# Performance work log

Measured on AMD Instinct MI355X. Metric: run time of the kernel, lower is better.

Reference implementation:

```python
import jax, jax.numpy as jnp
import numpy as np

DIM = 1024
DIM_HEAD = 64
HEADS = 16
INNER = DIM_HEAD * HEADS
SCALE = 8.0
EPS_LN = 1e-5
EPS_L2 = 1e-12


def _layernorm(x, gamma):
    mu = jnp.mean(x, axis=-1, keepdims=True)
    var = jnp.var(x, axis=-1, keepdims=True)
    return (x - mu) / jnp.sqrt(var + EPS_LN) * gamma  # beta is a zero buffer


def _l2norm(t):
    n = jnp.linalg.norm(t, axis=-1, keepdims=True)
    return t / jnp.maximum(n, EPS_L2)


def setup_inputs() -> dict:
    key = jax.random.key(0)
    ks = jax.random.split(key, 8)
    b, n = 4, 2048
    x = jax.random.normal(ks[0], (b, n, DIM), dtype=jnp.float32)
    context_mask = jax.random.randint(ks[1], (b, n), 0, 2) > 0
    gamma = jnp.ones((DIM,), dtype=jnp.float32)
    wq = jax.random.normal(ks[2], (DIM, INNER), dtype=jnp.float32) * 0.02
    wkv = jax.random.normal(ks[3], (DIM, 2 * INNER), dtype=jnp.float32) * 0.02
    null_kv = jax.random.normal(ks[4], (2, HEADS, 1, DIM_HEAD), dtype=jnp.float32)
    q_scale = jnp.ones((DIM_HEAD,), dtype=jnp.float32)
    k_scale = jnp.ones((DIM_HEAD,), dtype=jnp.float32)
    wo = jax.random.normal(ks[5], (INNER, DIM), dtype=jnp.float32) * 0.02
    return {"x": x, "context_mask": context_mask, "gamma": gamma, "wq": wq,
            "wkv": wkv, "null_kv": null_kv, "q_scale": q_scale,
            "k_scale": k_scale, "wo": wo}


def reference(x, context_mask, gamma, wq, wkv, null_kv, q_scale, k_scale, wo):
    b, n, _ = x.shape
    xn = _layernorm(x, gamma)
    q = xn @ wq                     # [b, n, inner]
    kv = xn @ wkv                   # self-attention: kv_input = x
    k, v = jnp.split(kv, 2, axis=-1)

    def split_heads(t):
        return t.reshape(b, n, HEADS, DIM_HEAD).transpose(0, 2, 1, 3)  # b h n d

    q, k, v = map(split_heads, (q, k, v))
    nk = jnp.broadcast_to(null_kv[0][None], (b, HEADS, 1, DIM_HEAD))
    nv = jnp.broadcast_to(null_kv[1][None], (b, HEADS, 1, DIM_HEAD))
    k = jnp.concatenate([nk, k], axis=2)  # b h (n+1) d
    v = jnp.concatenate([nv, v], axis=2)

    q = _l2norm(q) * q_scale
    k = _l2norm(k) * k_scale

    sim = jnp.einsum('bhid,bhjd->bhij', q, k) * SCALE  # b h n (n+1)
    mask = jnp.pad(context_mask, ((0, 0), (1, 0)), constant_values=True)  # null kv always visible
    mask_value = -jnp.finfo(sim.dtype).max
    sim = jnp.where(mask[:, None, None, :], sim, mask_value)

    attn = jax.nn.softmax(sim, axis=-1)
    out = jnp.einsum('bhij,bhjd->bhid', attn, v)
    out = out.transpose(0, 2, 1, 3).reshape(b, n, INNER)
    return out @ wo
```

## Files before the change

### kernel.cpp

```cpp
#include <hip/hip_runtime.h>

typedef unsigned short u16;
typedef unsigned int u32;
typedef unsigned long long u64;
typedef __bf16 bf16x8 __attribute__((ext_vector_type(8)));
typedef float f32x4 __attribute__((ext_vector_type(4)));

#define B_ 4
#define N_ 2048
#define D_ 1024
#define H_ 16
#define DH_ 64
#define NKP_ 2112
#define NKT_ 33

__device__ __forceinline__ float bf2f(u16 u) {
  union { u32 i; float f; } v; v.i = ((u32)u) << 16; return v.f;
}
__device__ __forceinline__ u16 f2bf(float f) {
  union { float f; u32 i; } v; v.f = f;
  u32 r = v.i + 0x7fffu + ((v.i >> 16) & 1u);
  return (u16)(r >> 16);
}
__device__ __forceinline__ u32 cvtpk(float a, float b) {
  u32 r;
  asm("v_cvt_pk_bf16_f32 %0, %1, %2" : "=v"(r) : "v"(a), "v"(b));
  return r;
}
__device__ __forceinline__ void load_lds16(const void* g, void* l) {
  __builtin_amdgcn_global_load_lds((const __attribute__((address_space(1))) void*)g,
                                   (__attribute__((address_space(3))) void*)l, 16, 0, 0);
}

__global__ __launch_bounds__(256) void ln_kernel(const float* __restrict__ x,
                                                 const float* __restrict__ gamma,
                                                 u16* __restrict__ xn) {
  int row = blockIdx.x;
  int tid = threadIdx.x, lane = tid & 63, wid = tid >> 6;
  const float4 v = ((const float4*)(x + (size_t)row * D_))[tid];
  float s  = v.x + v.y + v.z + v.w;
  float ss = v.x * v.x + v.y * v.y + v.z * v.z + v.w * v.w;
#pragma unroll
  for (int off = 1; off < 64; off <<= 1) {
    s  += __shfl_xor(s,  off, 64);
    ss += __shfl_xor(ss, off, 64);
  }
  __shared__ float rs[4], rss[4];
  if (lane == 0) { rs[wid] = s; rss[wid] = ss; }
  __syncthreads();
  float S  = rs[0] + rs[1] + rs[2] + rs[3];
  float SS = rss[0] + rss[1] + rss[2] + rss[3];
  float mean = S * (1.0f / D_);
  float var  = SS * (1.0f / D_) - mean * mean;
  float inv  = rsqrtf(var + 1e-5f);
  const float4 g = ((const float4*)gamma)[tid];
  u16* o = xn + (size_t)row * D_ + tid * 4;
  o[0] = f2bf((v.x - mean) * inv * g.x);
  o[1] = f2bf((v.y - mean) * inv * g.y);
  o[2] = f2bf((v.z - mean) * inv * g.z);
  o[3] = f2bf((v.w - mean) * inv * g.w);
}

__global__ __launch_bounds__(256) void wt_kernel(const float* __restrict__ W,
                                                 u16* __restrict__ WT,
                                                 int K, int N) {
  __shared__ float t[32][33];
  int tiles_n = N >> 5;
  int tk = blockIdx.x / tiles_n, tn = blockIdx.x % tiles_n;
  int tx = threadIdx.x & 31, ty = threadIdx.x >> 5;
  int k0 = tk << 5, n0 = tn << 5;
#pragma unroll
  for (int i = 0; i < 4; ++i)
    t[ty + i * 8][tx] = W[(size_t)(k0 + ty + i * 8) * N + n0 + tx];
  __syncthreads();
#pragma unroll
  for (int i = 0; i < 4; ++i)
    WT[(size_t)(n0 + ty + i * 8) * K + k0 + tx] = f2bf(t[tx][ty + i * 8]);
}

__global__ __launch_bounds__(256) void prep_kernel(const int* __restrict__ mask,
                                                   const float* __restrict__ qs,
                                                   const float* __restrict__ ksc,
                                                   const float* __restrict__ null_kv,
                                                   u16* __restrict__ Kb,
                                                   u16* __restrict__ Vt,
                                                   u64* __restrict__ km,
                                                   float* __restrict__ cb) {
  int bh = blockIdx.x, h = bh & 15;
  int tid = threadIdx.x, lane = tid & 63, wid = tid >> 6;
  if (wid == 0) {
    float kv = null_kv[h * 64 + lane];
    float ss = kv * kv;
#pragma unroll
    for (int off = 1; off < 64; off <<= 1) ss += __shfl_xor(ss, off, 64);
    float inv = 1.0f / fmaxf(sqrtf(ss), 1e-12f);
    Kb[((size_t)bh * NKP_ + 2048) * 64 + lane] = f2bf(kv * inv * ksc[lane]);
    Vt[((size_t)bh * 64 + lane) * NKP_ + 2048] = f2bf(null_kv[1024 + h * 64 + lane]);
  }
  for (int i = tid; i < 63 * 64; i += 256) {
    int r = i >> 6, c = i & 63;
    Kb[((size_t)bh * NKP_ + 2049 + r) * 64 + c] = 0;
  }
  for (int i = tid; i < 64 * 63; i += 256) {
    int d = i / 63, c = i % 63;
    Vt[((size_t)bh * 64 + d) * NKP_ + 2049 + c] = 0;
  }
  if (bh == 0) {
    if (tid < B_ * NKT_) {
      int b = tid / NKT_, kt = tid % NKT_;
      u64 m = 0;
      if (kt < 32) {
#pragma unroll 8
        for (int jj = 0; jj < 64; ++jj)
          m |= (u64)(mask[b * N_ + kt * 64 + jj] != 0) << jj;
      } else {
        m = 1ull;
      }
      km[tid] = m;
    }
    if (tid == 0) {
      float mw = 0.f;
      for (int i = 0; i < DH_; ++i) mw = fmaxf(mw, fabsf(qs[i] * ksc[i]));
      cb[0] = -8.0f * mw * 1.4426950408889634f;
    }
  }
}

template <int MODE>
__global__ __launch_bounds__(256) void gemm_bt(const u16* __restrict__ A,
                                               const u16* __restrict__ Bt,
                                               void* __restrict__ Cv,
                                               int M, int N, int K,
                                               const float* __restrict__ qs,
                                               u16* __restrict__ Vt) {
  __shared__ __attribute__((aligned(16))) u16 sm[2 * 128 * 64];
  u16* a_sm = sm;
  u16* b_sm = sm + 128 * 64;
  int tid = threadIdx.x, lane = tid & 63, wid = tid >> 6;
  int m0 = blockIdx.x * 128, n0 = blockIdx.y * 128;
  int wm = (wid >> 1) * 64, wn = (wid & 1) * 64;
  int sr = lane >> 3, sc = (lane & 7) * 8;
  int la = lane & 15, lk = (lane >> 4) * 8;
  f32x4 acc[4][4] = {};
  for (int k0 = 0; k0 < K; k0 += 64) {
    __syncthreads();
#pragma unroll
    for (int i = 0; i < 4; ++i) {
      int r = i * 32 + wid * 8;
      load_lds16(A  + (size_t)(m0 + r + sr) * K + k0 + sc, &a_sm[r * 64]);
      load_lds16(Bt + (size_t)(n0 + r + sr) * K + k0 + sc, &b_sm[r * 64]);
    }
    __syncthreads();
#pragma unroll
    for (int s = 0; s < 2; ++s) {
      bf16x8 af[4], bfr[4];
#pragma unroll
      for (int mf = 0; mf < 4; ++mf)
        af[mf] = *(const bf16x8*)&a_sm[(wm + mf * 16 + la) * 64 + s * 32 + lk];
#pragma unroll
      for (int nf = 0; nf < 4; ++nf)
        bfr[nf] = *(const bf16x8*)&b_sm[(wn + nf * 16 + la) * 64 + s * 32 + lk];
#pragma unroll
      for (int mf = 0; mf < 4; ++mf)
#pragma unroll
        for (int nf = 0; nf < 4; ++nf)
          acc[mf][nf] = __builtin_amdgcn_mfma_f32_16x16x32_bf16(af[mf], bfr[nf], acc[mf][nf], 0, 0, 0);
    }
  }
  int crow = (lane >> 4) * 4, ccol = lane & 15;

  if (MODE == 3) {
    int by = blockIdx.y;
    int rr0 = m0 + wm;
    int b = rr0 >> 11;
    int seq0 = rr0 & 2047;
    if (by < 8) {
      int h = by * 2 + (wn >> 6);
      float kscv[4];
#pragma unroll
      for (int nf = 0; nf < 4; ++nf) kscv[nf] = qs[nf * 16 + ccol];
      u16* kb = (u16*)Cv + ((size_t)(b * 16 + h) * NKP_) * 64;
#pragma unroll
      for (int mf = 0; mf < 4; ++mf) {
        float invr[4];
#pragma unroll
        for (int r = 0; r < 4; ++r) {
          float ss = 0.f;
#pragma unroll
          for (int nf = 0; nf < 4; ++nf) ss += acc[mf][nf][r] * acc[mf][nf][r];
#pragma unroll
          for (int off = 1; off < 16; off <<= 1) ss += __shfl_xor(ss, off, 64);
          invr[r] = 1.0f / fmaxf(sqrtf(ss), 1e-12f);
        }
#pragma unroll
        for (int nf = 0; nf < 4; ++nf)
#pragma unroll
          for (int r = 0; r < 4; ++r)
            kb[(size_t)(seq0 + mf * 16 + crow + r) * 64 + nf * 16 + ccol] =
                f2bf(acc[mf][nf][r] * invr[r] * kscv[nf]);
      }
    } else {
      int h = (by - 8) * 2 + (wn >> 6);
      __syncthreads();
      u16* tw = sm + wid * 4096;
#pragma unroll
      for (int mf = 0; mf < 4; ++mf)
#pragma unroll
        for (int nf = 0; nf < 4; ++nf) {
          int row = nf * 16 + ccol;
#pragma unroll
          for (int r = 0; r < 4; ++r)
            tw[row * 64 + ((mf * 16 + crow + r) ^ ((row & 7) * 8))] = f2bf(acc[mf][nf][r]);
        }
      u16* vb = Vt + ((size_t)(b * 16 + h) * 64) * NKP_;
      int dr = lane >> 3, kc = (lane & 7) * 8;
#pragma unroll
      for (int i = 0; i < 8; ++i) {
        int d = i * 8 + dr;
        bf16x8 vv = *(const bf16x8*)&tw[d * 64 + (kc ^ ((d & 7) * 8))];
        *(bf16x8*)(vb + (size_t)d * NKP_ + seq0 + kc) = vv;
      }
    }
    return;
  }

  float qsv[4];
  if (MODE == 2) {
#pragma unroll
    for (int nf = 0; nf < 4; ++nf) qsv[nf] = qs[nf * 16 + ccol];
  }
#pragma unroll
  for (int mf = 0; mf < 4; ++mf) {
    float invr[4];
    if (MODE == 2) {
#pragma unroll
      for (int r = 0; r < 4; ++r) {
        float ss = 0.f;
#pragma unroll
        for (int nf = 0; nf < 4; ++nf) ss += acc[mf][nf][r] * acc[mf][nf][r];
#pragma unroll
        for (int off = 1; off < 16; off <<= 1) ss += __shfl_xor(ss, off, 64);
        invr[r] = 1.0f / fmaxf(sqrtf(ss), 1e-12f);
      }
    }
#pragma unroll
    for (int nf = 0; nf < 4; ++nf) {
      int rr = m0 + wm + mf * 16 + crow;
      int cc = n0 + wn + nf * 16 + ccol;
      if (MODE == 1) {
        float* C = (float*)Cv;
#pragma unroll
        for (int r = 0; r < 4; ++r) C[(size_t)(rr + r) * N + cc] = acc[mf][nf][r];
      } else if (MODE == 0) {
        u16* C = (u16*)Cv;
#pragma unroll
        for (int r = 0; r < 4; ++r) C[(size_t)(rr + r) * N + cc] = f2bf(acc[mf][nf][r]);
      } else {
        u16* C = (u16*)Cv;
#pragma unroll
        for (int r = 0; r < 4; ++r)
          C[(size_t)(rr + r) * N + cc] = f2bf(acc[mf][nf][r] * invr[r] * qsv[nf]);
      }
    }
  }
}

__global__ __launch_bounds__(512) void attn_kernel(const u16* __restrict__ Q,
                                                   const u16* __restrict__ Kb,
                                                   const u16* __restrict__ Vt,
                                                   const u64* __restrict__ km,
                                                   const float* __restrict__ cb,
                                                   u16* __restrict__ O) {
  __shared__ __attribute__((aligned(16))) u16 k_sm[2][64 * 64];
  __shared__ __attribute__((aligned(16))) u16 v_sm[2][64 * 64];
  __shared__ __attribute__((aligned(16))) u16 p_sm[8][32 * 64];
  int tid = threadIdx.x, lane = tid & 63, wid = tid >> 6;
  int bh = blockIdx.x, b = bh >> 4, h = bh & 15;
  int q0 = blockIdx.y * 256 + wid * 32;
  int la = lane & 15, lk = (lane >> 4) * 8, crow = (lane >> 4) * 4;
  int swz = (la & 7) * 8;
  int sr = lane >> 3;
  int scz = ((lane & 7) ^ (lane >> 3)) * 8;

  bf16x8 aq[2][2];
#pragma unroll
  for (int qb = 0; qb < 2; ++qb) {
    const u16* qrow = Q + ((size_t)(b * N_) + q0 + qb * 16 + la) * D_ + h * DH_;
#pragma unroll
    for (int s = 0; s < 2; ++s) aq[qb][s] = *(const bf16x8*)(qrow + s * 32 + lk);
  }
  float l[2] = {0.f, 0.f};
  f32x4 o[2][4] = {};
  const u16* Kbh = Kb + (size_t)bh * NKP_ * 64;
  const u16* Vbh = Vt + (size_t)bh * 64 * NKP_;
  const u64* kmb = km + (size_t)b * NKT_;
  const float C1 = 11.541560327111707f;
  const float cbias = cb[0];

#define STAGE(bb, kt)                                                          \
  do {                                                                         \
    int key0_ = (kt) * 64;                                                     \
    int r_ = wid * 8;                                                          \
    load_lds16(Kbh + (size_t)(key0_ + r_ + sr) * 64 + scz, &k_sm[bb][r_ * 64]); \
    load_lds16(Vbh + (size_t)(r_ + sr) * NKP_ + key0_ + scz, &v_sm[bb][r_ * 64]); \
  } while (0)

  STAGE(0, 0);

  for (int kt = 0; kt < NKT_; ++kt) {
    int bb = kt & 1;
    __syncthreads();
    if (kt + 1 < NKT_) STAGE(bb ^ 1, kt + 1);
    u64 kmv = kmb[kt];

    f32x4 sacc[2][4] = {};
    __builtin_amdgcn_s_setprio(1);
#pragma unroll
    for (int nf = 0; nf < 4; ++nf) {
      bf16x8 bk0 = *(const bf16x8*)&k_sm[bb][(nf * 16 + la) * 64 + (lk ^ swz)];
      bf16x8 bk1 = *(const bf16x8*)&k_sm[bb][(nf * 16 + la) * 64 + ((32 + lk) ^ swz)];
#pragma unroll
      for (int qb = 0; qb < 2; ++qb) {
        sacc[qb][nf] = __builtin_amdgcn_mfma_f32_16x16x32_bf16(bk0, aq[qb][0], sacc[qb][nf], 0, 0, 0);
        sacc[qb][nf] = __builtin_amdgcn_mfma_f32_16x16x32_bf16(bk1, aq[qb][1], sacc[qb][nf], 0, 0, 0);
      }
    }
    __builtin_amdgcn_s_setprio(0);

#pragma unroll
    for (int nf = 0; nf < 4; ++nf) {
      u32 nib = ((u32)(kmv >> (nf * 16 + crow))) & 0xFu;
      int key = nf * 16 + crow;
#pragma unroll
      for (int qb = 0; qb < 2; ++qb) {
        float p0 = __builtin_amdgcn_exp2f(fmaf(sacc[qb][nf][0], C1, cbias));
        float p1 = __builtin_amdgcn_exp2f(fmaf(sacc[qb][nf][1], C1, cbias));
        float p2 = __builtin_amdgcn_exp2f(fmaf(sacc[qb][nf][2], C1, cbias));
        float p3 = __builtin_amdgcn_exp2f(fmaf(sacc[qb][nf][3], C1, cbias));
        p0 = (nib & 1u) ? p0 : 0.f;
        p1 = (nib & 2u) ? p1 : 0.f;
        p2 = (nib & 4u) ? p2 : 0.f;
        p3 = (nib & 8u) ? p3 : 0.f;
        l[qb] += (p0 + p1) + (p2 + p3);
        int row = qb * 16 + la;
        *(u32*)&p_sm[wid][row * 64 + (key ^ swz)] = cvtpk(p0, p1);
        *(u32*)&p_sm[wid][row * 64 + ((key + 2) ^ swz)] = cvtpk(p2, p3);
      }
    }

    __builtin_amdgcn_s_setprio(1);
#pragma unroll
    for (int s = 0; s < 2; ++s) {
      bf16x8 bv[4];
#pragma unroll
      for (int dt = 0; dt < 4; ++dt)
        bv[dt] = *(const bf16x8*)&v_sm[bb][(dt * 16 + la) * 64 + ((s * 32 + lk) ^ swz)];
#pragma unroll
      for (int qb = 0; qb < 2; ++qb) {
        bf16x8 ap = *(const bf16x8*)&p_sm[wid][(qb * 16 + la) * 64 + ((s * 32 + lk) ^ swz)];
#pragma unroll
        for (int dt = 0; dt < 4; ++dt)
          o[qb][dt] = __builtin_amdgcn_mfma_f32_16x16x32_bf16(ap, bv[dt], o[qb][dt], 0, 0, 0);
      }
    }
    __builtin_amdgcn_s_setprio(0);
  }
#undef STAGE

#pragma unroll
  for (int qb = 0; qb < 2; ++qb) {
    l[qb] += __shfl_xor(l[qb], 16, 64);
    l[qb] += __shfl_xor(l[qb], 32, 64);
#pragma unroll
    for (int r = 0; r < 4; ++r) {
      float lq = __shfl(l[qb], crow + r, 64);
      float inv = 1.0f / lq;
      int n = q0 + qb * 16 + crow + r;
      u16* ob = O + ((size_t)(b * N_) + n) * D_ + h * DH_;
#pragma unroll
      for (int dt = 0; dt < 4; ++dt) ob[dt * 16 + la] = f2bf(o[qb][dt][r] * inv);
    }
  }
}

extern "C" void kernel_launch(void* const* d_in, const int* in_sizes, int n_in,
                              void* d_out, int out_size, void* d_ws, size_t ws_size,
                              hipStream_t stream) {
  (void)in_sizes; (void)n_in; (void)out_size; (void)ws_size;
  const float* x     = (const float*)d_in[0];
  const int*   mask  = (const int*)d_in[1];
  const float* gamma = (const float*)d_in[2];
  const float* wq    = (const float*)d_in[3];
  const float* wkv   = (const float*)d_in[4];
  const float* nkv   = (const float*)d_in[5];
  const float* qs    = (const float*)d_in[6];
  const float* ksc   = (const float*)d_in[7];
  const float* wo    = (const float*)d_in[8];

  char* ws   = (char*)d_ws;
  u16* xn    = (u16*)(ws);
  u16* wqT   = (u16*)(ws + (16ull << 20));
  u16* wkvT  = (u16*)(ws + (18ull << 20));
  u16* woT   = (u16*)(ws + (22ull << 20));
  u16* Kb    = (u16*)(ws + (24ull << 20));
  u16* Vt    = (u16*)(ws + (41ull << 20));
  u64* kmask = (u64*)(ws + (58ull << 20));
  float* cb  = (float*)(ws + (58ull << 20) + 4096);
  u16* q_tmp = (u16*)d_out;
  u16* attn_out = xn;

  ln_kernel<<<B_ * N_, 256, 0, stream>>>(x, gamma, xn);
  wt_kernel<<<(1024 / 32) * (1024 / 32), 256, 0, stream>>>(wq, wqT, 1024, 1024);
  wt_kernel<<<(1024 / 32) * (2048 / 32), 256, 0, stream>>>(wkv, wkvT, 1024, 2048);
  wt_kernel<<<(1024 / 32) * (1024 / 32), 256, 0, stream>>>(wo, woT, 1024, 1024);
  prep_kernel<<<64, 256, 0, stream>>>(mask, qs, ksc, nkv, Kb, Vt, kmask, cb);
  gemm_bt<2><<<dim3(64, 8),  256, 0, stream>>>(xn, wqT,  q_tmp, 8192, 1024, 1024, qs, nullptr);
  gemm_bt<3><<<dim3(64, 16), 256, 0, stream>>>(xn, wkvT, Kb,    8192, 2048, 1024, ksc, Vt);
  attn_kernel<<<dim3(64, 8), 512, 0, stream>>>(q_tmp, Kb, Vt, kmask, cb, attn_out);
  gemm_bt<1><<<dim3(64, 8), 256, 0, stream>>>(attn_out, woT, (float*)d_out, 8192, 1024, 1024, nullptr, nullptr);
}
```

Baseline: 232.1 us.

## Keep attention probabilities in registers via lane permutes and shrink attention blocks

```diff
diff --git a/kernel.cpp b/kernel.cpp
--- a/kernel.cpp
+++ b/kernel.cpp
@@ -26,6 +26,12 @@
   u32 r;
   asm("v_cvt_pk_bf16_f32 %0, %1, %2" : "=v"(r) : "v"(a), "v"(b));
   return r;
+}
+__device__ __forceinline__ void swap32(u32& a, u32& b) {
+  asm volatile("v_permlane32_swap_b32 %0, %1" : "+v"(a), "+v"(b));
+}
+__device__ __forceinline__ u32 swz16(u32 x) {
+  return (u32)__builtin_amdgcn_ds_swizzle((int)x, 0x401F);
 }
 __device__ __forceinline__ void load_lds16(const void* g, void* l) {
   __builtin_amdgcn_global_load_lds((const __attribute__((address_space(1))) void*)g,
@@ -265,22 +271,22 @@
   }
 }
 
-__global__ __launch_bounds__(512) void attn_kernel(const u16* __restrict__ Q,
-                                                   const u16* __restrict__ Kb,
-                                                   const u16* __restrict__ Vt,
-                                                   const u64* __restrict__ km,
-                                                   const float* __restrict__ cb,
-                                                   u16* __restrict__ O) {
+__global__ __launch_bounds__(256, 4) void attn_kernel(const u16* __restrict__ Q,
+                                                      const u16* __restrict__ Kb,
+                                                      const u16* __restrict__ Vt,
+                                                      const u64* __restrict__ km,
+                                                      const float* __restrict__ cb,
+                                                      u16* __restrict__ O) {
   __shared__ __attribute__((aligned(16))) u16 k_sm[2][64 * 64];
   __shared__ __attribute__((aligned(16))) u16 v_sm[2][64 * 64];
-  __shared__ __attribute__((aligned(16))) u16 p_sm[8][32 * 64];
   int tid = threadIdx.x, lane = tid & 63, wid = tid >> 6;
   int bh = blockIdx.x, b = bh >> 4, h = bh & 15;
-  int q0 = blockIdx.y * 256 + wid * 32;
+  int q0 = blockIdx.y * 128 + wid * 32;
   int la = lane & 15, lk = (lane >> 4) * 8, crow = (lane >> 4) * 4;
   int swz = (la & 7) * 8;
   int sr = lane >> 3;
   int scz = ((lane & 7) ^ (lane >> 3)) * 8;
+  bool odd = (lane & 16) != 0;
 
   bf16x8 aq[2][2];
 #pragma unroll
@@ -300,9 +306,12 @@
 #define STAGE(bb, kt)                                                          \
   do {                                                                         \
     int key0_ = (kt) * 64;                                                     \
-    int r_ = wid * 8;                                                          \
-    load_lds16(Kbh + (size_t)(key0_ + r_ + sr) * 64 + scz, &k_sm[bb][r_ * 64]); \
-    load_lds16(Vbh + (size_t)(r_ + sr) * NKP_ + key0_ + scz, &v_sm[bb][r_ * 64]); \
+    _Pragma("unroll")                                                          \
+    for (int i_ = 0; i_ < 2; ++i_) {                                           \
+      int r_ = wid * 16 + i_ * 8;                                              \
+      load_lds16(Kbh + (size_t)(key0_ + r_ + sr) * 64 + scz, &k_sm[bb][r_ * 64]); \
+      load_lds16(Vbh + (size_t)(r_ + sr) * NKP_ + key0_ + scz, &v_sm[bb][r_ * 64]); \
+    }                                                                          \
   } while (0)
 
   STAGE(0, 0);
@@ -327,10 +336,10 @@
     }
     __builtin_amdgcn_s_setprio(0);
 
+    u32 w_[2][4][2];
 #pragma unroll
     for (int nf = 0; nf < 4; ++nf) {
       u32 nib = ((u32)(kmv >> (nf * 16 + crow))) & 0xFu;
-      int key = nf * 16 + crow;
 #pragma unroll
       for (int qb = 0; qb < 2; ++qb) {
         float p0 = __builtin_amdgcn_exp2f(fmaf(sacc[qb][nf][0], C1, cbias));
@@ -342,11 +351,27 @@
         p2 = (nib & 4u) ? p2 : 0.f;
         p3 = (nib & 8u) ? p3 : 0.f;
         l[qb] += (p0 + p1) + (p2 + p3);
-        int row = qb * 16 + la;
-        *(u32*)&p_sm[wid][row * 64 + (key ^ swz)] = cvtpk(p0, p1);
-        *(u32*)&p_sm[wid][row * 64 + ((key + 2) ^ swz)] = cvtpk(p2, p3);
-      }
-    }
+        w_[qb][nf][0] = cvtpk(p0, p1);
+        w_[qb][nf][1] = cvtpk(p2, p3);
+      }
+    }
+
+    union { u32 w[4]; bf16x8 v; } apu;
+    bf16x8 ap[2][2];
+#pragma unroll
+    for (int qb = 0; qb < 2; ++qb)
+#pragma unroll
+      for (int s = 0; s < 2; ++s) {
+#pragma unroll
+        for (int u = 0; u < 2; ++u) {
+          u32 a = w_[qb][2 * s][u], bsrc = w_[qb][2 * s + 1][u];
+          swap32(a, bsrc);
+          u32 sa = swz16(a), sb = swz16(bsrc);
+          apu.w[u]     = odd ? sb   : a;
+          apu.w[u + 2] = odd ? bsrc : sa;
+        }
+        ap[qb][s] = apu.v;
+      }
 
     __builtin_amdgcn_s_setprio(1);
 #pragma unroll
@@ -356,12 +381,10 @@
       for (int dt = 0; dt < 4; ++dt)
         bv[dt] = *(const bf16x8*)&v_sm[bb][(dt * 16 + la) * 64 + ((s * 32 + lk) ^ swz)];
 #pragma unroll
-      for (int qb = 0; qb < 2; ++qb) {
-        bf16x8 ap = *(const bf16x8*)&p_sm[wid][(qb * 16 + la) * 64 + ((s * 32 + lk) ^ swz)];
+      for (int qb = 0; qb < 2; ++qb)
 #pragma unroll
         for (int dt = 0; dt < 4; ++dt)
-          o[qb][dt] = __builtin_amdgcn_mfma_f32_16x16x32_bf16(ap, bv[dt], o[qb][dt], 0, 0, 0);
-      }
+          o[qb][dt] = __builtin_amdgcn_mfma_f32_16x16x32_bf16(ap[qb][s], bv[dt], o[qb][dt], 0, 0, 0);
     }
     __builtin_amdgcn_s_setprio(0);
   }
@@ -416,6 +439,6 @@
   prep_kernel<<<64, 256, 0, stream>>>(mask, qs, ksc, nkv, Kb, Vt, kmask, cb);
   gemm_bt<2><<<dim3(64, 8),  256, 0, stream>>>(xn, wqT,  q_tmp, 8192, 1024, 1024, qs, nullptr);
   gemm_bt<3><<<dim3(64, 16), 256, 0, stream>>>(xn, wkvT, Kb,    8192, 2048, 1024, ksc, Vt);
-  attn_kernel<<<dim3(64, 8), 512, 0, stream>>>(q_tmp, Kb, Vt, kmask, cb, attn_out);
+  attn_kernel<<<dim3(64, 16), 256, 0, stream>>>(q_tmp, Kb, Vt, kmask, cb, attn_out);
   gemm_bt<1><<<dim3(64, 8), 256, 0, stream>>>(attn_out, woT, (float*)d_out, 8192, 1024, 1024, nullptr, nullptr);
 }
```

After: 241.0 us. +3.8%, slower.

## Fold key mask into zeroed K/V rows and subtract masked mass from softmax denominator

Applied to the files above, without the earlier changes.

```diff
diff --git a/kernel.cpp b/kernel.cpp
--- a/kernel.cpp
+++ b/kernel.cpp
@@ -84,8 +84,8 @@
                                                    const float* __restrict__ null_kv,
                                                    u16* __restrict__ Kb,
                                                    u16* __restrict__ Vt,
-                                                   u64* __restrict__ km,
                                                    float* __restrict__ cb) {
+  __shared__ int cnts[4];
   int bh = blockIdx.x, h = bh & 15;
   int tid = threadIdx.x, lane = tid & 63, wid = tid >> 6;
   if (wid == 0) {
@@ -106,22 +106,25 @@
     Vt[((size_t)bh * 64 + d) * NKP_ + 2049 + c] = 0;
   }
   if (bh == 0) {
-    if (tid < B_ * NKT_) {
-      int b = tid / NKT_, kt = tid % NKT_;
-      u64 m = 0;
-      if (kt < 32) {
-#pragma unroll 8
-        for (int jj = 0; jj < 64; ++jj)
-          m |= (u64)(mask[b * N_ + kt * 64 + jj] != 0) << jj;
-      } else {
-        m = 1ull;
-      }
-      km[tid] = m;
-    }
+    if (tid < 4) cnts[tid] = 0;
+    __syncthreads();
+    int c0 = 0, c1 = 0, c2 = 0, c3 = 0;
+    for (int i = tid; i < B_ * N_; i += 256) {
+      int z = (mask[i] == 0);
+      int b = i >> 11;
+      if (b == 0) c0 += z; else if (b == 1) c1 += z; else if (b == 2) c2 += z; else c3 += z;
+    }
+    atomicAdd(&cnts[0], c0); atomicAdd(&cnts[1], c1);
+    atomicAdd(&cnts[2], c2); atomicAdd(&cnts[3], c3);
+    __syncthreads();
     if (tid == 0) {
       float mw = 0.f;
       for (int i = 0; i < DH_; ++i) mw = fmaxf(mw, fabsf(qs[i] * ksc[i]));
-      cb[0] = -8.0f * mw * 1.4426950408889634f;
+      float cbias = -8.0f * mw * 1.4426950408889634f;
+      cb[0] = cbias;
+      float e = __builtin_amdgcn_exp2f(cbias);
+#pragma unroll
+      for (int b = 0; b < 4; ++b) cb[1 + b] = (float)(cnts[b] + 63) * e;
     }
   }
 }
@@ -132,7 +135,8 @@
                                                void* __restrict__ Cv,
                                                int M, int N, int K,
                                                const float* __restrict__ qs,
-                                               u16* __restrict__ Vt) {
+                                               u16* __restrict__ Vt,
+                                               const int* __restrict__ Mask) {
   __shared__ __attribute__((aligned(16))) u16 sm[2 * 128 * 64];
   u16* a_sm = sm;
   u16* b_sm = sm + 128 * 64;
@@ -174,6 +178,7 @@
     int rr0 = m0 + wm;
     int b = rr0 >> 11;
     int seq0 = rr0 & 2047;
+    const int* mrow = Mask + b * N_ + seq0;
     if (by < 8) {
       int h = by * 2 + (wn >> 6);
       float kscv[4];
@@ -182,7 +187,7 @@
       u16* kb = (u16*)Cv + ((size_t)(b * 16 + h) * NKP_) * 64;
 #pragma unroll
       for (int mf = 0; mf < 4; ++mf) {
-        float invr[4];
+        float invr[4]; int mvv[4];
 #pragma unroll
         for (int r = 0; r < 4; ++r) {
           float ss = 0.f;
@@ -191,27 +196,33 @@
 #pragma unroll
           for (int off = 1; off < 16; off <<= 1) ss += __shfl_xor(ss, off, 64);
           invr[r] = 1.0f / fmaxf(sqrtf(ss), 1e-12f);
+          mvv[r] = mrow[mf * 16 + crow + r];
         }
 #pragma unroll
         for (int nf = 0; nf < 4; ++nf)
 #pragma unroll
           for (int r = 0; r < 4; ++r)
             kb[(size_t)(seq0 + mf * 16 + crow + r) * 64 + nf * 16 + ccol] =
-                f2bf(acc[mf][nf][r] * invr[r] * kscv[nf]);
+                f2bf(mvv[r] ? acc[mf][nf][r] * invr[r] * kscv[nf] : 0.f);
       }
     } else {
       int h = (by - 8) * 2 + (wn >> 6);
       __syncthreads();
       u16* tw = sm + wid * 4096;
 #pragma unroll
-      for (int mf = 0; mf < 4; ++mf)
+      for (int mf = 0; mf < 4; ++mf) {
+        int mvv[4];
+#pragma unroll
+        for (int r = 0; r < 4; ++r) mvv[r] = mrow[mf * 16 + crow + r];
 #pragma unroll
         for (int nf = 0; nf < 4; ++nf) {
           int row = nf * 16 + ccol;
 #pragma unroll
           for (int r = 0; r < 4; ++r)
-            tw[row * 64 + ((mf * 16 + crow + r) ^ ((row & 7) * 8))] = f2bf(acc[mf][nf][r]);
+            tw[row * 64 + ((mf * 16 + crow + r) ^ ((row & 7) * 8))] =
+                f2bf(mvv[r] ? acc[mf][nf][r] : 0.f);
         }
+      }
       u16* vb = Vt + ((size_t)(b * 16 + h) * 64) * NKP_;
       int dr = lane >> 3, kc = (lane & 7) * 8;
 #pragma unroll
@@ -268,7 +279,6 @@
 __global__ __launch_bounds__(512) void attn_kernel(const u16* __restrict__ Q,
                                                    const u16* __restrict__ Kb,
                                                    const u16* __restrict__ Vt,
-                                                   const u64* __restrict__ km,
                                                    const float* __restrict__ cb,
                                                    u16* __restrict__ O) {
   __shared__ __attribute__((aligned(16))) u16 k_sm[2][64 * 64];
@@ -293,9 +303,9 @@
   f32x4 o[2][4] = {};
   const u16* Kbh = Kb + (size_t)bh * NKP_ * 64;
   const u16* Vbh = Vt + (size_t)bh * 64 * NKP_;
-  const u64* kmb = km + (size_t)b * NKT_;
   const float C1 = 11.541560327111707f;
   const float cbias = cb[0];
+  const float lsub = cb[1 + b];
 
 #define STAGE(bb, kt)                                                          \
   do {                                                                         \
@@ -307,11 +317,11 @@
 
   STAGE(0, 0);
 
+#pragma unroll 2
   for (int kt = 0; kt < NKT_; ++kt) {
     int bb = kt & 1;
     __syncthreads();
     if (kt + 1 < NKT_) STAGE(bb ^ 1, kt + 1);
-    u64 kmv = kmb[kt];
 
     f32x4 sacc[2][4] = {};
     __builtin_amdgcn_s_setprio(1);
@@ -329,7 +339,6 @@
 
 #pragma unroll
     for (int nf = 0; nf < 4; ++nf) {
-      u32 nib = ((u32)(kmv >> (nf * 16 + crow))) & 0xFu;
       int key = nf * 16 + crow;
 #pragma unroll
       for (int qb = 0; qb < 2; ++qb) {
@@ -337,14 +346,11 @@
         float p1 = __builtin_amdgcn_exp2f(fmaf(sacc[qb][nf][1], C1, cbias));
         float p2 = __builtin_amdgcn_exp2f(fmaf(sacc[qb][nf][2], C1, cbias));
         float p3 = __builtin_amdgcn_exp2f(fmaf(sacc[qb][nf][3], C1, cbias));
-        p0 = (nib & 1u) ? p0 : 0.f;
-        p1 = (nib & 2u) ? p1 : 0.f;
-        p2 = (nib & 4u) ? p2 : 0.f;
-        p3 = (nib & 8u) ? p3 : 0.f;
         l[qb] += (p0 + p1) + (p2 + p3);
-        int row = qb * 16 + la;
-        *(u32*)&p_sm[wid][row * 64 + (key ^ swz)] = cvtpk(p0, p1);
-        *(u32*)&p_sm[wid][row * 64 + ((key + 2) ^ swz)] = cvtpk(p2, p3);
+        uint2 pw;
+        pw.x = cvtpk(p0, p1);
+        pw.y = cvtpk(p2, p3);
+        *(uint2*)&p_sm[wid][(qb * 16 + la) * 64 + (key ^ swz)] = pw;
       }
     }
 
@@ -373,7 +379,7 @@
     l[qb] += __shfl_xor(l[qb], 32, 64);
 #pragma unroll
     for (int r = 0; r < 4; ++r) {
-      float lq = __shfl(l[qb], crow + r, 64);
+      float lq = __shfl(l[qb], crow + r, 64) - lsub;
       float inv = 1.0f / lq;
       int n = q0 + qb * 16 + crow + r;
       u16* ob = O + ((size_t)(b * N_) + n) * D_ + h * DH_;
@@ -404,8 +410,7 @@
   u16* woT   = (u16*)(ws + (22ull << 20));
   u16* Kb    = (u16*)(ws + (24ull << 20));
   u16* Vt    = (u16*)(ws + (41ull << 20));
-  u64* kmask = (u64*)(ws + (58ull << 20));
-  float* cb  = (float*)(ws + (58ull << 20) + 4096);
+  float* cb  = (float*)(ws + (58ull << 20));
   u16* q_tmp = (u16*)d_out;
   u16* attn_out = xn;
 
@@ -413,9 +418,9 @@
   wt_kernel<<<(1024 / 32) * (1024 / 32), 256, 0, stream>>>(wq, wqT, 1024, 1024);
   wt_kernel<<<(1024 / 32) * (2048 / 32), 256, 0, stream>>>(wkv, wkvT, 1024, 2048);
   wt_kernel<<<(1024 / 32) * (1024 / 32), 256, 0, stream>>>(wo, woT, 1024, 1024);
-  prep_kernel<<<64, 256, 0, stream>>>(mask, qs, ksc, nkv, Kb, Vt, kmask, cb);
-  gemm_bt<2><<<dim3(64, 8),  256, 0, stream>>>(xn, wqT,  q_tmp, 8192, 1024, 1024, qs, nullptr);
-  gemm_bt<3><<<dim3(64, 16), 256, 0, stream>>>(xn, wkvT, Kb,    8192, 2048, 1024, ksc, Vt);
-  attn_kernel<<<dim3(64, 8), 512, 0, stream>>>(q_tmp, Kb, Vt, kmask, cb, attn_out);
-  gemm_bt<1><<<dim3(64, 8), 256, 0, stream>>>(attn_out, woT, (float*)d_out, 8192, 1024, 1024, nullptr, nullptr);
-}
+  prep_kernel<<<64, 256, 0, stream>>>(mask, qs, ksc, nkv, Kb, Vt, cb);
+  gemm_bt<2><<<dim3(64, 8),  256, 0, stream>>>(xn, wqT,  q_tmp, 8192, 1024, 1024, qs, nullptr, nullptr);
+  gemm_bt<3><<<dim3(64, 16), 256, 0, stream>>>(xn, wkvT, Kb,    8192, 2048, 1024, ksc, Vt, mask);
+  attn_kernel<<<dim3(64, 8), 512, 0, stream>>>(q_tmp, Kb, Vt, cb, attn_out);
+  gemm_bt<1><<<dim3(64, 8), 256, 0, stream>>>(attn_out, woT, (float*)d_out, 8192, 1024, 1024, nullptr, nullptr, nullptr);
+}
```

After: 231.7 us. About the same (-0.2%).
